# Optimization experiments

Measured on AMD Instinct MI355X. Metric: run time of the kernel, lower is better.

Reference implementation:

```python
import jax, jax.numpy as jnp
import numpy as np

C = 256
NUM_HEADS = 4
REDUCTION = 4
RED = C // REDUCTION           # 64
HEAD_DIM = RED // NUM_HEADS    # 16
SCALE = HEAD_DIM ** -0.5
LN_EPS = 1e-5


def setup_inputs() -> dict:
    key = jax.random.key(0)
    ks = jax.random.split(key, 9)
    B, H, W = 2, 64, 64
    x = jax.random.normal(ks[0], (B, C, H, W), dtype=jnp.float32)
    # LayerNorm params
    norm_w = jnp.ones((C,), jnp.float32)
    norm_b = jnp.zeros((C,), jnp.float32)
    # Linear weights (torch layout: [out, in]), y = x @ W.T
    qkv_w = jax.random.normal(ks[1], (3 * RED, C), jnp.float32) * (C ** -0.5)
    out_w = jax.random.normal(ks[2], (C, RED), jnp.float32) * (RED ** -0.5)
    # 1x1 conv weights, stored as [out_c, in_c]
    conv1_w = jax.random.normal(ks[3], (C // 2, C), jnp.float32) * (C ** -0.5)
    conv1_b = jax.random.normal(ks[4], (C // 2,), jnp.float32) * 0.01
    conv2_w = jax.random.normal(ks[5], (1, C // 2), jnp.float32) * ((C // 2) ** -0.5)
    conv2_b = jax.random.normal(ks[6], (1,), jnp.float32) * 0.01
    gamma = jnp.ones((1,), jnp.float32) * 0.5  # nonzero so output depends on attention
    return {"x": x, "norm_w": norm_w, "norm_b": norm_b, "qkv_w": qkv_w,
            "out_w": out_w, "conv1_w": conv1_w, "conv1_b": conv1_b,
            "conv2_w": conv2_w, "conv2_b": conv2_b, "gamma": gamma}


def reference(x, norm_w, norm_b, qkv_w, out_w, conv1_w, conv1_b, conv2_w, conv2_b, gamma):
    B, C_, H, W = x.shape
    N = H * W
    # [B, N, C]
    xf = x.reshape(B, C_, N).transpose(0, 2, 1)
    # LayerNorm over channel dim
    mu = jnp.mean(xf, axis=-1, keepdims=True)
    var = jnp.mean(jnp.square(xf - mu), axis=-1, keepdims=True)
    xn = (xf - mu) * jax.lax.rsqrt(var + LN_EPS) * norm_w + norm_b
    # QKV projection -> [B, N, 3*RED]
    qkv = jnp.einsum('bnc,oc->bno', xn, qkv_w)
    q, k, v = jnp.split(qkv, 3, axis=-1)
    def heads(t):  # [B, N, RED] -> [B, h, N, d]
        return t.reshape(B, N, NUM_HEADS, HEAD_DIM).transpose(0, 2, 1, 3)
    q, k, v = heads(q), heads(k), heads(v)
    attn = jax.nn.softmax(jnp.einsum('bhnd,bhmd->bhnm', q, k) * SCALE, axis=-1)
    # dynamic weight branch: two 1x1 convs on raw x
    d1 = jax.nn.relu(jnp.einsum('oc,bchw->bohw', conv1_w, x) + conv1_b[None, :, None, None])
    dyn = (jnp.einsum('oc,bchw->bohw', conv2_w, d1) + conv2_b[None, :, None, None])  # [B,1,H,W]
    dyn = dyn.reshape(B, 1, N)  # broadcast over heads
    # per-query row scaling of attention
    attn = attn * dyn[:, :, :, None]
    out = jnp.einsum('bhnm,bhmd->bhnd', attn, v)            # [B,h,N,d]
    out = out.transpose(0, 2, 1, 3).reshape(B, N, RED)      # [B,N,RED]
    out = jnp.einsum('bnr,cr->bnc', out, out_w)             # [B,N,C]
    out = out.transpose(0, 2, 1).reshape(B, C_, H, W)
    return jax.nn.sigmoid(gamma[0] * out + x)
```

## Files before the change

### kernel.cpp

```cpp
#include <hip/hip_runtime.h>
#include <cstdint>
#include <cstddef>

#define LOG2E 1.44269504088896340736f

typedef float  f32x16 __attribute__((ext_vector_type(16)));
typedef __bf16 bf16x8 __attribute__((ext_vector_type(8)));

union BF8 { bf16x8 v; uint u[4]; ushort us[8]; };

__device__ __forceinline__ uint pack_bf(float a, float b) {
    uint ua = __float_as_uint(a) + 0x8000u;
    uint ub = __float_as_uint(b) + 0x8000u;
    return __builtin_amdgcn_perm(ub, ua, 0x07060302u);
}
__device__ __forceinline__ float bf_lo(uint u) { return __uint_as_float(u << 16); }
__device__ __forceinline__ float bf_hi(uint u) { return __uint_as_float(u & 0xFFFF0000u); }

__global__ __launch_bounds__(256) void convert_w_kernel(
    const float* __restrict__ qkv_w, const float* __restrict__ c1w,
    const float* __restrict__ out_w,
    ushort* __restrict__ qkvw_b, ushort* __restrict__ c1w_b, ushort* __restrict__ ow_b)
{
    const int g = (blockIdx.x * 256 + threadIdx.x) * 4;
    const float* src; ushort* dst; int off; float sc = 1.f;
    if (g < 49152)      { src = qkv_w; dst = qkvw_b; off = g;
                          if (g < 16384) sc = 0.25f * LOG2E; }
    else if (g < 81920) { src = c1w;   dst = c1w_b;  off = g - 49152; }
    else                { src = out_w; dst = ow_b;   off = g - 81920; }
    float4 v = *(const float4*)(src + off);
    uint2 pk;
    pk.x = pack_bf(v.x * sc, v.y * sc);
    pk.y = pack_bf(v.z * sc, v.w * sc);
    *(uint2*)(dst + off) = pk;
}

__global__ __launch_bounds__(256) void ln_cast_kernel(
    const float* __restrict__ x, const float* __restrict__ nw, const float* __restrict__ nb,
    ushort* __restrict__ xnb, ushort* __restrict__ xrb)
{
    __shared__ uint  xp[32 * 144];
    __shared__ float red1[256], red2[256];
    __shared__ float muS[32], rsS[32];

    const int t  = threadIdx.x;
    const int b  = blockIdx.x >> 7;
    const int n0 = (blockIdx.x & 127) * 32;
    const int j  = t & 31;
    const int cg = t >> 5;
    const size_t xb = (size_t)b * 256 * 4096 + n0 + j;

    float v[32];
    #pragma unroll
    for (int i = 0; i < 32; ++i) v[i] = x[xb + (size_t)(cg * 32 + i) * 4096];
    float s1 = 0.f, s2 = 0.f;
    #pragma unroll
    for (int i = 0; i < 32; ++i) { s1 += v[i]; s2 += v[i] * v[i]; }
    #pragma unroll
    for (int i = 0; i < 16; ++i)
        xp[j * 144 + cg * 16 + i] = pack_bf(v[2 * i], v[2 * i + 1]);
    red1[t] = s1; red2[t] = s2;
    __syncthreads();
    if (t < 32) {
        float a = 0.f, q = 0.f;
        #pragma unroll
        for (int g2 = 0; g2 < 8; ++g2) { a += red1[g2 * 32 + t]; q += red2[g2 * 32 + t]; }
        float mu  = a * (1.f / 256.f);
        float var = q * (1.f / 256.f) - mu * mu;
        muS[t] = mu; rsS[t] = rsqrtf(fmaxf(var, 0.f) + 1e-5f);
    }
    __syncthreads();

    for (int it = 0; it < 4; ++it) {
        int lin = it * 256 + t;
        int px = lin >> 5, q = lin & 31;
        uint4 raw = *(uint4*)&xp[px * 144 + q * 4];
        size_t row = (size_t)blockIdx.x * 32 + px;
        *(uint4*)(xrb + row * 256 + q * 8) = raw;

        float mu = muS[px], rs = rsS[px];
        const float4 w0 = *(const float4*)(nw + q * 8);
        const float4 w1 = *(const float4*)(nw + q * 8 + 4);
        const float4 b0 = *(const float4*)(nb + q * 8);
        const float4 b1 = *(const float4*)(nb + q * 8 + 4);
        float e0 = (bf_lo(raw.x) - mu) * rs * w0.x + b0.x;
        float e1 = (bf_hi(raw.x) - mu) * rs * w0.y + b0.y;
        float e2 = (bf_lo(raw.y) - mu) * rs * w0.z + b0.z;
        float e3 = (bf_hi(raw.y) - mu) * rs * w0.w + b0.w;
        float e4 = (bf_lo(raw.z) - mu) * rs * w1.x + b1.x;
        float e5 = (bf_hi(raw.z) - mu) * rs * w1.y + b1.y;
        float e6 = (bf_lo(raw.w) - mu) * rs * w1.z + b1.z;
        float e7 = (bf_hi(raw.w) - mu) * rs * w1.w + b1.w;
        uint4 o;
        o.x = pack_bf(e0, e1); o.y = pack_bf(e2, e3);
        o.z = pack_bf(e4, e5); o.w = pack_bf(e6, e7);
        *(uint4*)(xnb + row * 256 + q * 8) = o;
    }
}

__global__ __launch_bounds__(256) void qkvconv_kernel(
    const ushort* __restrict__ xnb, const ushort* __restrict__ xrb,
    const ushort* __restrict__ qkvw_b, const ushort* __restrict__ c1w_b,
    const float* __restrict__ c1b, const float* __restrict__ c2w,
    const float* __restrict__ c2b,
    ushort* __restrict__ Qb, ushort* __restrict__ Kb, ushort* __restrict__ Vsw,
    float* __restrict__ dynb)
{
    __shared__ float trans[4][32 * 33];
    const int t    = threadIdx.x;
    const int w    = t >> 6;
    const int lane = t & 63;
    const int m    = lane & 31;
    const int h    = lane >> 5;
    const int pg   = blockIdx.x;
    const int b    = pg >> 7;
    const int n0   = (pg & 127) * 32;
    float* tr = trans[w];

    if (w < 3) {
        const ushort* bp  = xnb + ((size_t)pg * 32 + m) * 256 + h * 8;
        const ushort* ap0 = qkvw_b + ((size_t)(w * 64 + m)) * 256 + h * 8;
        const ushort* ap1 = ap0 + 32 * 256;
        f32x16 acc0, acc1;
        #pragma unroll
        for (int i = 0; i < 16; ++i) { acc0[i] = 0.f; acc1[i] = 0.f; }
        #pragma unroll 4
        for (int ks = 0; ks < 16; ++ks) {
            bf16x8 bf = *(const bf16x8*)(bp  + ks * 16);
            bf16x8 a0 = *(const bf16x8*)(ap0 + ks * 16);
            bf16x8 a1 = *(const bf16x8*)(ap1 + ks * 16);
            acc0 = __builtin_amdgcn_mfma_f32_32x32x16_bf16(a0, bf, acc0, 0, 0, 0);
            acc1 = __builtin_amdgcn_mfma_f32_32x32x16_bf16(a1, bf, acc1, 0, 0, 0);
        }
        for (int ti = 0; ti < 2; ++ti) {
            const f32x16& A = ti ? acc1 : acc0;
            #pragma unroll
            for (int r = 0; r < 16; ++r)
                tr[((r & 3) + 8 * (r >> 2) + 4 * h) * 33 + m] = A[r];
            if (w < 2) {
                ushort* dst = (w == 0) ? Qb : Kb;
                #pragma unroll
                for (int it = 0; it < 2; ++it) {
                    int unit = it * 2 + h;
                    int hl = unit >> 1, half = unit & 1;
                    float v0 = tr[(hl * 16 + half * 8 + 0) * 33 + m];
                    float v1 = tr[(hl * 16 + half * 8 + 1) * 33 + m];
                    float v2 = tr[(hl * 16 + half * 8 + 2) * 33 + m];
                    float v3 = tr[(hl * 16 + half * 8 + 3) * 33 + m];
                    float v4 = tr[(hl * 16 + half * 8 + 4) * 33 + m];
                    float v5 = tr[(hl * 16 + half * 8 + 5) * 33 + m];
                    float v6 = tr[(hl * 16 + half * 8 + 6) * 33 + m];
                    float v7 = tr[(hl * 16 + half * 8 + 7) * 33 + m];
                    uint4 pk;
                    pk.x = pack_bf(v0, v1); pk.y = pack_bf(v2, v3);
                    pk.z = pack_bf(v4, v5); pk.w = pack_bf(v6, v7);
                    int head = ti * 2 + hl;
                    *(uint4*)(dst + ((size_t)(b * 4 + head) * 4096 + n0 + m) * 16 + half * 8) = pk;
                }
            } else {
                int d = lane & 15, u = lane >> 4;
                #pragma unroll
                for (int it = 0; it < 4; ++it) {
                    int unit = it * 4 + u;
                    int hl = unit >> 3, sg = unit & 7;
                    float v0 = tr[(hl * 16 + d) * 33 + sg * 4 + 0];
                    float v1 = tr[(hl * 16 + d) * 33 + sg * 4 + 1];
                    float v2 = tr[(hl * 16 + d) * 33 + sg * 4 + 2];
                    float v3 = tr[(hl * 16 + d) * 33 + sg * 4 + 3];
                    uint2 pk; pk.x = pack_bf(v0, v1); pk.y = pack_bf(v2, v3);
                    int head = ti * 2 + hl;
                    *(uint2*)(Vsw + (((size_t)(b * 4 + head) * 1024 + (pg & 127) * 8 + sg) * 16 + d) * 4) = pk;
                }
            }
        }
    } else {
        const ushort* bp = xrb + ((size_t)pg * 32 + m) * 256 + h * 8;
        f32x16 acc[4];
        #pragma unroll
        for (int ti = 0; ti < 4; ++ti)
            #pragma unroll
            for (int i = 0; i < 16; ++i) acc[ti][i] = 0.f;
        #pragma unroll 2
        for (int ks = 0; ks < 16; ++ks) {
            bf16x8 bf = *(const bf16x8*)(bp + ks * 16);
            #pragma unroll
            for (int ti = 0; ti < 4; ++ti) {
                bf16x8 a = *(const bf16x8*)(c1w_b + ((size_t)(ti * 32 + m)) * 256 + ks * 16 + h * 8);
                acc[ti] = __builtin_amdgcn_mfma_f32_32x32x16_bf16(a, bf, acc[ti], 0, 0, 0);
            }
        }
        float partial = 0.f;
        for (int ti = 0; ti < 4; ++ti) {
            #pragma unroll
            for (int r = 0; r < 16; ++r)
                tr[((r & 3) + 8 * (r >> 2) + 4 * h) * 33 + m] = acc[ti][r];
            #pragma unroll
            for (int i = 0; i < 16; ++i) {
                int og = ti * 32 + h * 16 + i;
                partial += fmaxf(tr[(h * 16 + i) * 33 + m] + c1b[og], 0.f) * c2w[og];
            }
        }
        float tot = partial + __shfl_xor(partial, 32);
        if (lane < 32) dynb[(size_t)b * 4096 + n0 + m] = c2b[0] + tot;
    }
}

__global__ __launch_bounds__(256) void attn_kernel(
    const ushort* __restrict__ Qb, const ushort* __restrict__ Kb,
    const ushort* __restrict__ Vsw, float* __restrict__ AO2)
{
    const int t   = threadIdx.x;
    const int lid = t & 63;
    const int w   = t >> 6;
    const int c   = lid & 31;
    const int h   = lid >> 5;

    const int bi = blockIdx.x;
    const int kb = bi & 1;
    const int qb = (bi >> 1) & 31;
    const int bh = bi >> 6;
    const int nq = qb * 128 + w * 32;

    const bf16x8 qf = *(const bf16x8*)(Qb + ((size_t)bh * 4096 + nq + c) * 16 + h * 8);

    f32x16 oacc, zf;
    #pragma unroll
    for (int i = 0; i < 16; ++i) { oacc[i] = 0.f; zf[i] = 0.f; }

    const ushort* kp = Kb + ((size_t)bh * 4096 + kb * 2048 + c) * 16 + h * 8;
    const ushort* vb = Vsw + (size_t)bh * 65536 + ((size_t)kb * 512 + h) * 64 + c * 4;

    #pragma unroll 2
    for (int ch = 0; ch < 64; ++ch) {
        const bf16x8 kf = *(const bf16x8*)kp;
        f32x16 s = __builtin_amdgcn_mfma_f32_32x32x16_bf16(kf, qf, zf, 0, 0, 0);

        BF8 p1, p2;
        #pragma unroll
        for (int jj = 0; jj < 4; ++jj) {
            p1.u[jj] = pack_bf(__builtin_amdgcn_exp2f(s[2*jj]),   __builtin_amdgcn_exp2f(s[2*jj+1]));
            p2.u[jj] = pack_bf(__builtin_amdgcn_exp2f(s[8+2*jj]), __builtin_amdgcn_exp2f(s[8+2*jj+1]));
        }

        BF8 a1, a2;
        if (c < 16) {
            const uint2 g1 = *(const uint2*)(vb);
            const uint2 g2 = *(const uint2*)(vb + 128);
            const uint2 g3 = *(const uint2*)(vb + 256);
            const uint2 g4 = *(const uint2*)(vb + 384);
            a1.u[0] = g1.x; a1.u[1] = g1.y; a1.u[2] = g2.x; a1.u[3] = g2.y;
            a2.u[0] = g3.x; a2.u[1] = g3.y; a2.u[2] = g4.x; a2.u[3] = g4.y;
        } else {
            const uint f = (c == 16) ? 0x3F803F80u : 0u;
            a1.u[0] = a1.u[1] = a1.u[2] = a1.u[3] = f;
            a2.u[0] = a2.u[1] = a2.u[2] = a2.u[3] = f;
        }

        oacc = __builtin_amdgcn_mfma_f32_32x32x16_bf16(a1.v, p1.v, oacc, 0, 0, 0);
        oacc = __builtin_amdgcn_mfma_f32_32x32x16_bf16(a2.v, p2.v, oacc, 0, 0, 0);

        kp += 512; vb += 512;
    }

    float* ao = AO2 + ((size_t)(kb * 8 + bh) * 4096 + nq + c) * 20;
    float4 s0; s0.x = oacc[0]; s0.y = oacc[1]; s0.z = oacc[2]; s0.w = oacc[3];
    float4 s1; s1.x = oacc[4]; s1.y = oacc[5]; s1.z = oacc[6]; s1.w = oacc[7];
    *(float4*)(ao + 4 * h)     = s0;
    *(float4*)(ao + 8 + 4 * h) = s1;
    if (h == 0) ao[16] = oacc[8];
}

__global__ __launch_bounds__(256) void final_kernel(
    const float* __restrict__ AO2, const float* __restrict__ dynb,
    const ushort* __restrict__ ow_b, const float* __restrict__ x,
    const float* __restrict__ gamma, float* __restrict__ out)
{
    __shared__ float trans[4][32 * 33];
    const int t    = threadIdx.x;
    const int w    = t >> 6;
    const int lane = t & 63;
    const int m    = lane & 31;
    const int h    = lane >> 5;
    const int pg   = blockIdx.x;
    const int b    = pg >> 7;
    const int n0   = (pg & 127) * 32;
    float* tr = trans[w];

    const float dyn_px = dynb[(size_t)b * 4096 + n0 + m];
    const ushort* a0p = ow_b + ((size_t)(w * 64 + m)) * 64 + h * 8;
    const ushort* a1p = a0p + 32 * 64;

    f32x16 acc0, acc1;
    #pragma unroll
    for (int i = 0; i < 16; ++i) { acc0[i] = 0.f; acc1[i] = 0.f; }

    #pragma unroll
    for (int ks = 0; ks < 4; ++ks) {
        const float* r0 = AO2 + ((size_t)(b * 4 + ks) * 4096 + n0 + m) * 20;
        const float* r1 = r0 + (size_t)8 * 4096 * 20;
        float l   = r0[16] + r1[16];
        float fac = dyn_px / l;
        float4 u0 = *(const float4*)(r0 + h * 8);
        float4 u1 = *(const float4*)(r0 + h * 8 + 4);
        float4 t0 = *(const float4*)(r1 + h * 8);
        float4 t1 = *(const float4*)(r1 + h * 8 + 4);
        float e0 = (u0.x + t0.x) * fac, e1 = (u0.y + t0.y) * fac;
        float e2 = (u0.z + t0.z) * fac, e3 = (u0.w + t0.w) * fac;
        float e4 = (u1.x + t1.x) * fac, e5 = (u1.y + t1.y) * fac;
        float e6 = (u1.z + t1.z) * fac, e7 = (u1.w + t1.w) * fac;
        BF8 bfr;
        bfr.u[0] = pack_bf(e0, e1); bfr.u[1] = pack_bf(e2, e3);
        bfr.u[2] = pack_bf(e4, e5); bfr.u[3] = pack_bf(e6, e7);
        bf16x8 af0 = *(const bf16x8*)(a0p + ks * 16);
        bf16x8 af1 = *(const bf16x8*)(a1p + ks * 16);
        acc0 = __builtin_amdgcn_mfma_f32_32x32x16_bf16(af0, bfr.v, acc0, 0, 0, 0);
        acc1 = __builtin_amdgcn_mfma_f32_32x32x16_bf16(af1, bfr.v, acc1, 0, 0, 0);
    }

    const float g = gamma[0];
    for (int ti = 0; ti < 2; ++ti) {
        const f32x16& A = ti ? acc1 : acc0;
        #pragma unroll
        for (int r = 0; r < 16; ++r)
            tr[((r & 3) + 8 * (r >> 2) + 4 * h) * 33 + m] = A[r];
        int ob = w * 64 + ti * 32;
        #pragma unroll 4
        for (int it = 0; it < 16; ++it) {
            int o = it * 2 + h;
            float vv = tr[o * 33 + m];
            size_t idx = ((size_t)b * 256 + ob + o) * 4096 + n0 + m;
            float z = g * vv + x[idx];
            out[idx] = 1.f / (1.f + __builtin_amdgcn_exp2f(-z * LOG2E));
        }
    }
}

extern "C" void kernel_launch(void* const* d_in, const int* in_sizes, int n_in,
                              void* d_out, int out_size, void* d_ws, size_t ws_size,
                              hipStream_t stream)
{
    const float* x      = (const float*)d_in[0];
    const float* norm_w = (const float*)d_in[1];
    const float* norm_b = (const float*)d_in[2];
    const float* qkv_w  = (const float*)d_in[3];
    const float* out_w  = (const float*)d_in[4];
    const float* c1w    = (const float*)d_in[5];
    const float* c1b    = (const float*)d_in[6];
    const float* c2w    = (const float*)d_in[7];
    const float* c2b    = (const float*)d_in[8];
    const float* gamma  = (const float*)d_in[9];

    char* ws = (char*)d_ws;
    ushort* Qb     = (ushort*)ws;
    ushort* Kb     = Qb + 524288;
    ushort* Vsw    = Kb + 524288;
    ushort* qkvw_b = Vsw + 524288;
    ushort* c1w_b  = qkvw_b + 49152;
    ushort* ow_b   = c1w_b + 32768;
    float*  dynb   = (float*)(ws + 3342336);
    ushort* xnb    = (ushort*)(ws + 3375104);
    ushort* xrb    = xnb + 2097152;
    float*  AO2    = (float*)(ws + 3375104);

    hipLaunchKernelGGL(convert_w_kernel, dim3(96), dim3(256), 0, stream,
                       qkv_w, c1w, out_w, qkvw_b, c1w_b, ow_b);
    hipLaunchKernelGGL(ln_cast_kernel, dim3(256), dim3(256), 0, stream,
                       x, norm_w, norm_b, xnb, xrb);
    hipLaunchKernelGGL(qkvconv_kernel, dim3(256), dim3(256), 0, stream,
                       xnb, xrb, qkvw_b, c1w_b, c1b, c2w, c2b, Qb, Kb, Vsw, dynb);
    hipLaunchKernelGGL(attn_kernel, dim3(512), dim3(256), 0, stream,
                       Qb, Kb, Vsw, AO2);
    hipLaunchKernelGGL(final_kernel, dim3(256), dim3(256), 0, stream,
                       AO2, dynb, ow_b, x, gamma, (float*)d_out);
}
```

Before: 139.3 us.

## Fold weight conversion into LN kernel, split qkvconv into single-wave blocks, truncate P packing

Weight-to-bf16 conversion now runs in extra blocks appended to the LayerNorm/cast kernel, removing one kernel launch. The qkv/conv kernel is restructured from 256-thread blocks with four role-specialized waves into 1024 single-wave blocks, each taking one role, to spread work across more CUs. Attention probabilities are packed to bf16 by truncation instead of round-to-nearest, saving ALU work in the inner loop. The truncation adds a small downward bias in the softmax numerators.

```diff
diff --git a/kernel.cpp b/kernel.cpp
--- a/kernel.cpp
+++ b/kernel.cpp
@@ -14,38 +14,42 @@
     uint ub = __float_as_uint(b) + 0x8000u;
     return __builtin_amdgcn_perm(ub, ua, 0x07060302u);
 }
+__device__ __forceinline__ uint pack_bf_trunc(float a, float b) {
+    return __builtin_amdgcn_perm(__float_as_uint(b), __float_as_uint(a), 0x07060302u);
+}
 __device__ __forceinline__ float bf_lo(uint u) { return __uint_as_float(u << 16); }
 __device__ __forceinline__ float bf_hi(uint u) { return __uint_as_float(u & 0xFFFF0000u); }
 
-__global__ __launch_bounds__(256) void convert_w_kernel(
-    const float* __restrict__ qkv_w, const float* __restrict__ c1w,
-    const float* __restrict__ out_w,
-    ushort* __restrict__ qkvw_b, ushort* __restrict__ c1w_b, ushort* __restrict__ ow_b)
-{
-    const int g = (blockIdx.x * 256 + threadIdx.x) * 4;
-    const float* src; ushort* dst; int off; float sc = 1.f;
-    if (g < 49152)      { src = qkv_w; dst = qkvw_b; off = g;
-                          if (g < 16384) sc = 0.25f * LOG2E; }
-    else if (g < 81920) { src = c1w;   dst = c1w_b;  off = g - 49152; }
-    else                { src = out_w; dst = ow_b;   off = g - 81920; }
-    float4 v = *(const float4*)(src + off);
-    uint2 pk;
-    pk.x = pack_bf(v.x * sc, v.y * sc);
-    pk.y = pack_bf(v.z * sc, v.w * sc);
-    *(uint2*)(dst + off) = pk;
-}
-
 __global__ __launch_bounds__(256) void ln_cast_kernel(
     const float* __restrict__ x, const float* __restrict__ nw, const float* __restrict__ nb,
-    ushort* __restrict__ xnb, ushort* __restrict__ xrb)
+    const float* __restrict__ qkv_w, const float* __restrict__ c1w, const float* __restrict__ out_w,
+    ushort* __restrict__ xnb, ushort* __restrict__ xrb,
+    ushort* __restrict__ qkvw_b, ushort* __restrict__ c1w_b, ushort* __restrict__ ow_b)
 {
     __shared__ uint  xp[32 * 144];
     __shared__ float red1[256], red2[256];
     __shared__ float muS[32], rsS[32];
 
     const int t  = threadIdx.x;
-    const int b  = blockIdx.x >> 7;
-    const int n0 = (blockIdx.x & 127) * 32;
+    const int bi = blockIdx.x;
+
+    if (bi >= 256) {
+        const int g = ((bi - 256) * 256 + t) * 4;
+        const float* src; ushort* dst; int off; float sc = 1.f;
+        if (g < 49152)      { src = qkv_w; dst = qkvw_b; off = g;
+                              if (g < 16384) sc = 0.25f * LOG2E; }
+        else if (g < 81920) { src = c1w;   dst = c1w_b;  off = g - 49152; }
+        else                { src = out_w; dst = ow_b;   off = g - 81920; }
+        float4 v = *(const float4*)(src + off);
+        uint2 pk;
+        pk.x = pack_bf(v.x * sc, v.y * sc);
+        pk.y = pack_bf(v.z * sc, v.w * sc);
+        *(uint2*)(dst + off) = pk;
+        return;
+    }
+
+    const int b  = bi >> 7;
+    const int n0 = (bi & 127) * 32;
     const int j  = t & 31;
     const int cg = t >> 5;
     const size_t xb = (size_t)b * 256 * 4096 + n0 + j;
@@ -75,7 +79,7 @@
         int lin = it * 256 + t;
         int px = lin >> 5, q = lin & 31;
         uint4 raw = *(uint4*)&xp[px * 144 + q * 4];
-        size_t row = (size_t)blockIdx.x * 32 + px;
+        size_t row = (size_t)bi * 32 + px;
         *(uint4*)(xrb + row * 256 + q * 8) = raw;
 
         float mu = muS[px], rs = rsS[px];
@@ -98,7 +102,7 @@
     }
 }
 
-__global__ __launch_bounds__(256) void qkvconv_kernel(
+__global__ __launch_bounds__(64) void qkvconv_kernel(
     const ushort* __restrict__ xnb, const ushort* __restrict__ xrb,
     const ushort* __restrict__ qkvw_b, const ushort* __restrict__ c1w_b,
     const float* __restrict__ c1b, const float* __restrict__ c2w,
@@ -106,20 +110,19 @@
     ushort* __restrict__ Qb, ushort* __restrict__ Kb, ushort* __restrict__ Vsw,
     float* __restrict__ dynb)
 {
-    __shared__ float trans[4][32 * 33];
-    const int t    = threadIdx.x;
-    const int w    = t >> 6;
-    const int lane = t & 63;
-    const int m    = lane & 31;
-    const int h    = lane >> 5;
-    const int pg   = blockIdx.x;
-    const int b    = pg >> 7;
-    const int n0   = (pg & 127) * 32;
-    float* tr = trans[w];
-
-    if (w < 3) {
+    __shared__ float tr[32 * 33];
+    const int t  = threadIdx.x;
+    const int m  = t & 31;
+    const int h  = t >> 5;
+    const int bi = blockIdx.x;
+    const int j  = bi & 3;
+    const int pg = bi >> 2;
+    const int b  = pg >> 7;
+    const int n0 = (pg & 127) * 32;
+
+    if (j < 3) {
         const ushort* bp  = xnb + ((size_t)pg * 32 + m) * 256 + h * 8;
-        const ushort* ap0 = qkvw_b + ((size_t)(w * 64 + m)) * 256 + h * 8;
+        const ushort* ap0 = qkvw_b + ((size_t)(j * 64 + m)) * 256 + h * 8;
         const ushort* ap1 = ap0 + 32 * 256;
         f32x16 acc0, acc1;
         #pragma unroll
@@ -137,8 +140,8 @@
             #pragma unroll
             for (int r = 0; r < 16; ++r)
                 tr[((r & 3) + 8 * (r >> 2) + 4 * h) * 33 + m] = A[r];
-            if (w < 2) {
-                ushort* dst = (w == 0) ? Qb : Kb;
+            if (j < 2) {
+                ushort* dst = (j == 0) ? Qb : Kb;
                 #pragma unroll
                 for (int it = 0; it < 2; ++it) {
                     int unit = it * 2 + h;
@@ -158,7 +161,7 @@
                     *(uint4*)(dst + ((size_t)(b * 4 + head) * 4096 + n0 + m) * 16 + half * 8) = pk;
                 }
             } else {
-                int d = lane & 15, u = lane >> 4;
+                int d = t & 15, u = t >> 4;
                 #pragma unroll
                 for (int it = 0; it < 4; ++it) {
                     int unit = it * 4 + u;
@@ -201,7 +204,7 @@
             }
         }
         float tot = partial + __shfl_xor(partial, 32);
-        if (lane < 32) dynb[(size_t)b * 4096 + n0 + m] = c2b[0] + tot;
+        if (t < 32) dynb[(size_t)b * 4096 + n0 + m] = c2b[0] + tot;
     }
 }
 
@@ -238,8 +241,8 @@
         BF8 p1, p2;
         #pragma unroll
         for (int jj = 0; jj < 4; ++jj) {
-            p1.u[jj] = pack_bf(__builtin_amdgcn_exp2f(s[2*jj]),   __builtin_amdgcn_exp2f(s[2*jj+1]));
-            p2.u[jj] = pack_bf(__builtin_amdgcn_exp2f(s[8+2*jj]), __builtin_amdgcn_exp2f(s[8+2*jj+1]));
+            p1.u[jj] = pack_bf_trunc(__builtin_amdgcn_exp2f(s[2*jj]),   __builtin_amdgcn_exp2f(s[2*jj+1]));
+            p2.u[jj] = pack_bf_trunc(__builtin_amdgcn_exp2f(s[8+2*jj]), __builtin_amdgcn_exp2f(s[8+2*jj+1]));
         }
 
         BF8 a1, a2;
@@ -362,11 +365,9 @@
     ushort* xrb    = xnb + 2097152;
     float*  AO2    = (float*)(ws + 3375104);
 
-    hipLaunchKernelGGL(convert_w_kernel, dim3(96), dim3(256), 0, stream,
-                       qkv_w, c1w, out_w, qkvw_b, c1w_b, ow_b);
-    hipLaunchKernelGGL(ln_cast_kernel, dim3(256), dim3(256), 0, stream,
-                       x, norm_w, norm_b, xnb, xrb);
-    hipLaunchKernelGGL(qkvconv_kernel, dim3(256), dim3(256), 0, stream,
+    hipLaunchKernelGGL(ln_cast_kernel, dim3(352), dim3(256), 0, stream,
+                       x, norm_w, norm_b, qkv_w, c1w, out_w, xnb, xrb, qkvw_b, c1w_b, ow_b);
+    hipLaunchKernelGGL(qkvconv_kernel, dim3(1024), dim3(64), 0, stream,
                        xnb, xrb, qkvw_b, c1w_b, c1b, c2w, c2b, Qb, Kb, Vsw, dynb);
     hipLaunchKernelGGL(attn_kernel, dim3(512), dim3(256), 0, stream,
                        Qb, Kb, Vsw, AO2);
```

New measurement: 141.6 us. Within noise of the previous version (+1.6%).

## Fuse weight conversion, LayerNorm and QKV/conv projections into one pre-kernel

Applied to the files above, without the earlier changes.

Merges the weight-conversion, LayerNorm/cast and QKV/conv1 projection kernels into a single kernel. Normalized and raw activations stay in shared memory instead of a global round trip, and fp32 weights are converted to bf16 on the fly inside the MFMA loops, including in the final kernel. This removes two launches and the intermediate global buffers, at the cost of redundant per-block weight conversion and larger fp32 weight loads. The attention softmax also switches to truncating bf16 packing to save an add per element.

```diff
diff --git a/kernel.cpp b/kernel.cpp
--- a/kernel.cpp
+++ b/kernel.cpp
@@ -14,124 +14,103 @@
     uint ub = __float_as_uint(b) + 0x8000u;
     return __builtin_amdgcn_perm(ub, ua, 0x07060302u);
 }
-__device__ __forceinline__ float bf_lo(uint u) { return __uint_as_float(u << 16); }
-__device__ __forceinline__ float bf_hi(uint u) { return __uint_as_float(u & 0xFFFF0000u); }
-
-__global__ __launch_bounds__(256) void convert_w_kernel(
+__device__ __forceinline__ uint pack_bf_trunc(float a, float b) {
+    return __builtin_amdgcn_perm(__float_as_uint(b), __float_as_uint(a), 0x07060302u);
+}
+
+__global__ __launch_bounds__(256) void fused_pre_kernel(
+    const float* __restrict__ x, const float* __restrict__ nw, const float* __restrict__ nb,
     const float* __restrict__ qkv_w, const float* __restrict__ c1w,
-    const float* __restrict__ out_w,
-    ushort* __restrict__ qkvw_b, ushort* __restrict__ c1w_b, ushort* __restrict__ ow_b)
-{
-    const int g = (blockIdx.x * 256 + threadIdx.x) * 4;
-    const float* src; ushort* dst; int off; float sc = 1.f;
-    if (g < 49152)      { src = qkv_w; dst = qkvw_b; off = g;
-                          if (g < 16384) sc = 0.25f * LOG2E; }
-    else if (g < 81920) { src = c1w;   dst = c1w_b;  off = g - 49152; }
-    else                { src = out_w; dst = ow_b;   off = g - 81920; }
-    float4 v = *(const float4*)(src + off);
-    uint2 pk;
-    pk.x = pack_bf(v.x * sc, v.y * sc);
-    pk.y = pack_bf(v.z * sc, v.w * sc);
-    *(uint2*)(dst + off) = pk;
-}
-
-__global__ __launch_bounds__(256) void ln_cast_kernel(
-    const float* __restrict__ x, const float* __restrict__ nw, const float* __restrict__ nb,
-    ushort* __restrict__ xnb, ushort* __restrict__ xrb)
-{
-    __shared__ uint  xp[32 * 144];
-    __shared__ float red1[256], red2[256];
-    __shared__ float muS[32], rsS[32];
-
-    const int t  = threadIdx.x;
-    const int b  = blockIdx.x >> 7;
-    const int n0 = (blockIdx.x & 127) * 32;
-    const int j  = t & 31;
-    const int cg = t >> 5;
-    const size_t xb = (size_t)b * 256 * 4096 + n0 + j;
-
-    float v[32];
-    #pragma unroll
-    for (int i = 0; i < 32; ++i) v[i] = x[xb + (size_t)(cg * 32 + i) * 4096];
-    float s1 = 0.f, s2 = 0.f;
-    #pragma unroll
-    for (int i = 0; i < 32; ++i) { s1 += v[i]; s2 += v[i] * v[i]; }
-    #pragma unroll
-    for (int i = 0; i < 16; ++i)
-        xp[j * 144 + cg * 16 + i] = pack_bf(v[2 * i], v[2 * i + 1]);
-    red1[t] = s1; red2[t] = s2;
-    __syncthreads();
-    if (t < 32) {
-        float a = 0.f, q = 0.f;
-        #pragma unroll
-        for (int g2 = 0; g2 < 8; ++g2) { a += red1[g2 * 32 + t]; q += red2[g2 * 32 + t]; }
-        float mu  = a * (1.f / 256.f);
-        float var = q * (1.f / 256.f) - mu * mu;
-        muS[t] = mu; rsS[t] = rsqrtf(fmaxf(var, 0.f) + 1e-5f);
-    }
-    __syncthreads();
-
-    for (int it = 0; it < 4; ++it) {
-        int lin = it * 256 + t;
-        int px = lin >> 5, q = lin & 31;
-        uint4 raw = *(uint4*)&xp[px * 144 + q * 4];
-        size_t row = (size_t)blockIdx.x * 32 + px;
-        *(uint4*)(xrb + row * 256 + q * 8) = raw;
-
-        float mu = muS[px], rs = rsS[px];
-        const float4 w0 = *(const float4*)(nw + q * 8);
-        const float4 w1 = *(const float4*)(nw + q * 8 + 4);
-        const float4 b0 = *(const float4*)(nb + q * 8);
-        const float4 b1 = *(const float4*)(nb + q * 8 + 4);
-        float e0 = (bf_lo(raw.x) - mu) * rs * w0.x + b0.x;
-        float e1 = (bf_hi(raw.x) - mu) * rs * w0.y + b0.y;
-        float e2 = (bf_lo(raw.y) - mu) * rs * w0.z + b0.z;
-        float e3 = (bf_hi(raw.y) - mu) * rs * w0.w + b0.w;
-        float e4 = (bf_lo(raw.z) - mu) * rs * w1.x + b1.x;
-        float e5 = (bf_hi(raw.z) - mu) * rs * w1.y + b1.y;
-        float e6 = (bf_lo(raw.w) - mu) * rs * w1.z + b1.z;
-        float e7 = (bf_hi(raw.w) - mu) * rs * w1.w + b1.w;
-        uint4 o;
-        o.x = pack_bf(e0, e1); o.y = pack_bf(e2, e3);
-        o.z = pack_bf(e4, e5); o.w = pack_bf(e6, e7);
-        *(uint4*)(xnb + row * 256 + q * 8) = o;
-    }
-}
-
-__global__ __launch_bounds__(256) void qkvconv_kernel(
-    const ushort* __restrict__ xnb, const ushort* __restrict__ xrb,
-    const ushort* __restrict__ qkvw_b, const ushort* __restrict__ c1w_b,
-    const float* __restrict__ c1b, const float* __restrict__ c2w,
-    const float* __restrict__ c2b,
+    const float* __restrict__ c1b, const float* __restrict__ c2w, const float* __restrict__ c2b,
     ushort* __restrict__ Qb, ushort* __restrict__ Kb, ushort* __restrict__ Vsw,
     float* __restrict__ dynb)
 {
+    __shared__ uint  xpn[32 * 144];
+    __shared__ uint  xpr[32 * 144];
     __shared__ float trans[4][32 * 33];
-    const int t    = threadIdx.x;
+    __shared__ float red1[256], red2[256];
+    __shared__ float muS[32], rsS[32];
+    __shared__ float nwS[256], nbS[256];
+
+    const int t  = threadIdx.x;
+    const int pg = blockIdx.x;
+    const int b  = pg >> 7;
+    const int n0 = (pg & 127) * 32;
+
+    {
+        const int j  = t & 31;
+        const int cg = t >> 5;
+        const size_t xb = (size_t)b * 256 * 4096 + n0 + j;
+        nwS[t] = nw[t]; nbS[t] = nb[t];
+
+        float v[32];
+        #pragma unroll
+        for (int i = 0; i < 32; ++i) v[i] = x[xb + (size_t)(cg * 32 + i) * 4096];
+        float s1 = 0.f, s2 = 0.f;
+        #pragma unroll
+        for (int i = 0; i < 32; ++i) { s1 += v[i]; s2 += v[i] * v[i]; }
+        #pragma unroll
+        for (int i = 0; i < 16; ++i)
+            xpr[j * 144 + cg * 16 + i] = pack_bf(v[2 * i], v[2 * i + 1]);
+        red1[t] = s1; red2[t] = s2;
+        __syncthreads();
+        if (t < 32) {
+            float a = 0.f, q = 0.f;
+            #pragma unroll
+            for (int g2 = 0; g2 < 8; ++g2) { a += red1[g2 * 32 + t]; q += red2[g2 * 32 + t]; }
+            float mu  = a * (1.f / 256.f);
+            float var = q * (1.f / 256.f) - mu * mu;
+            muS[t] = mu; rsS[t] = rsqrtf(fmaxf(var, 0.f) + 1e-5f);
+        }
+        __syncthreads();
+        float mu = muS[j], rs = rsS[j];
+        #pragma unroll
+        for (int i = 0; i < 16; ++i) {
+            int c0 = cg * 32 + 2 * i;
+            float e0 = (v[2 * i]     - mu) * rs * nwS[c0]     + nbS[c0];
+            float e1 = (v[2 * i + 1] - mu) * rs * nwS[c0 + 1] + nbS[c0 + 1];
+            xpn[j * 144 + cg * 16 + i] = pack_bf(e0, e1);
+        }
+        __syncthreads();
+    }
+
     const int w    = t >> 6;
     const int lane = t & 63;
     const int m    = lane & 31;
     const int h    = lane >> 5;
-    const int pg   = blockIdx.x;
-    const int b    = pg >> 7;
-    const int n0   = (pg & 127) * 32;
     float* tr = trans[w];
 
     if (w < 3) {
-        const ushort* bp  = xnb + ((size_t)pg * 32 + m) * 256 + h * 8;
-        const ushort* ap0 = qkvw_b + ((size_t)(w * 64 + m)) * 256 + h * 8;
-        const ushort* ap1 = ap0 + 32 * 256;
+        const uint*  bp  = xpn + m * 144 + h * 4;
+        const float* w0p = qkv_w + (size_t)(w * 64 + m) * 256 + h * 8;
+        const float* w1p = w0p + 32 * 256;
+        const float sc = (w == 0) ? (0.25f * LOG2E) : 1.f;
+
         f32x16 acc0, acc1;
         #pragma unroll
         for (int i = 0; i < 16; ++i) { acc0[i] = 0.f; acc1[i] = 0.f; }
+
         #pragma unroll 4
         for (int ks = 0; ks < 16; ++ks) {
-            bf16x8 bf = *(const bf16x8*)(bp  + ks * 16);
-            bf16x8 a0 = *(const bf16x8*)(ap0 + ks * 16);
-            bf16x8 a1 = *(const bf16x8*)(ap1 + ks * 16);
-            acc0 = __builtin_amdgcn_mfma_f32_32x32x16_bf16(a0, bf, acc0, 0, 0, 0);
-            acc1 = __builtin_amdgcn_mfma_f32_32x32x16_bf16(a1, bf, acc1, 0, 0, 0);
-        }
+            uint4 bu = *(const uint4*)(bp + ks * 8);
+            BF8 bfr; bfr.u[0] = bu.x; bfr.u[1] = bu.y; bfr.u[2] = bu.z; bfr.u[3] = bu.w;
+            float4 a00 = *(const float4*)(w0p + ks * 16);
+            float4 a01 = *(const float4*)(w0p + ks * 16 + 4);
+            float4 a10 = *(const float4*)(w1p + ks * 16);
+            float4 a11 = *(const float4*)(w1p + ks * 16 + 4);
+            BF8 af0, af1;
+            af0.u[0] = pack_bf(a00.x * sc, a00.y * sc);
+            af0.u[1] = pack_bf(a00.z * sc, a00.w * sc);
+            af0.u[2] = pack_bf(a01.x * sc, a01.y * sc);
+            af0.u[3] = pack_bf(a01.z * sc, a01.w * sc);
+            af1.u[0] = pack_bf(a10.x * sc, a10.y * sc);
+            af1.u[1] = pack_bf(a10.z * sc, a10.w * sc);
+            af1.u[2] = pack_bf(a11.x * sc, a11.y * sc);
+            af1.u[3] = pack_bf(a11.z * sc, a11.w * sc);
+            acc0 = __builtin_amdgcn_mfma_f32_32x32x16_bf16(af0.v, bfr.v, acc0, 0, 0, 0);
+            acc1 = __builtin_amdgcn_mfma_f32_32x32x16_bf16(af1.v, bfr.v, acc1, 0, 0, 0);
+        }
+
         for (int ti = 0; ti < 2; ++ti) {
             const f32x16& A = ti ? acc1 : acc0;
             #pragma unroll
@@ -174,7 +153,7 @@
             }
         }
     } else {
-        const ushort* bp = xrb + ((size_t)pg * 32 + m) * 256 + h * 8;
+        const uint* bp = xpr + m * 144 + h * 4;
         f32x16 acc[4];
         #pragma unroll
         for (int ti = 0; ti < 4; ++ti)
@@ -182,11 +161,17 @@
             for (int i = 0; i < 16; ++i) acc[ti][i] = 0.f;
         #pragma unroll 2
         for (int ks = 0; ks < 16; ++ks) {
-            bf16x8 bf = *(const bf16x8*)(bp + ks * 16);
+            uint4 bu = *(const uint4*)(bp + ks * 8);
+            BF8 bfr; bfr.u[0] = bu.x; bfr.u[1] = bu.y; bfr.u[2] = bu.z; bfr.u[3] = bu.w;
             #pragma unroll
             for (int ti = 0; ti < 4; ++ti) {
-                bf16x8 a = *(const bf16x8*)(c1w_b + ((size_t)(ti * 32 + m)) * 256 + ks * 16 + h * 8);
-                acc[ti] = __builtin_amdgcn_mfma_f32_32x32x16_bf16(a, bf, acc[ti], 0, 0, 0);
+                const float* wp = c1w + (size_t)(ti * 32 + m) * 256 + ks * 16 + h * 8;
+                float4 a0 = *(const float4*)(wp);
+                float4 a1 = *(const float4*)(wp + 4);
+                BF8 af;
+                af.u[0] = pack_bf(a0.x, a0.y); af.u[1] = pack_bf(a0.z, a0.w);
+                af.u[2] = pack_bf(a1.x, a1.y); af.u[3] = pack_bf(a1.z, a1.w);
+                acc[ti] = __builtin_amdgcn_mfma_f32_32x32x16_bf16(af.v, bfr.v, acc[ti], 0, 0, 0);
             }
         }
         float partial = 0.f;
@@ -238,8 +223,8 @@
         BF8 p1, p2;
         #pragma unroll
         for (int jj = 0; jj < 4; ++jj) {
-            p1.u[jj] = pack_bf(__builtin_amdgcn_exp2f(s[2*jj]),   __builtin_amdgcn_exp2f(s[2*jj+1]));
-            p2.u[jj] = pack_bf(__builtin_amdgcn_exp2f(s[8+2*jj]), __builtin_amdgcn_exp2f(s[8+2*jj+1]));
+            p1.u[jj] = pack_bf_trunc(__builtin_amdgcn_exp2f(s[2*jj]),   __builtin_amdgcn_exp2f(s[2*jj+1]));
+            p2.u[jj] = pack_bf_trunc(__builtin_amdgcn_exp2f(s[8+2*jj]), __builtin_amdgcn_exp2f(s[8+2*jj+1]));
         }
 
         BF8 a1, a2;
@@ -272,7 +257,7 @@
 
 __global__ __launch_bounds__(256) void final_kernel(
     const float* __restrict__ AO2, const float* __restrict__ dynb,
-    const ushort* __restrict__ ow_b, const float* __restrict__ x,
+    const float* __restrict__ out_w, const float* __restrict__ x,
     const float* __restrict__ gamma, float* __restrict__ out)
 {
     __shared__ float trans[4][32 * 33];
@@ -287,8 +272,8 @@
     float* tr = trans[w];
 
     const float dyn_px = dynb[(size_t)b * 4096 + n0 + m];
-    const ushort* a0p = ow_b + ((size_t)(w * 64 + m)) * 64 + h * 8;
-    const ushort* a1p = a0p + 32 * 64;
+    const float* a0p = out_w + (size_t)(w * 64 + m) * 64 + h * 8;
+    const float* a1p = a0p + 32 * 64;
 
     f32x16 acc0, acc1;
     #pragma unroll
@@ -311,10 +296,19 @@
         BF8 bfr;
         bfr.u[0] = pack_bf(e0, e1); bfr.u[1] = pack_bf(e2, e3);
         bfr.u[2] = pack_bf(e4, e5); bfr.u[3] = pack_bf(e6, e7);
-        bf16x8 af0 = *(const bf16x8*)(a0p + ks * 16);
-        bf16x8 af1 = *(const bf16x8*)(a1p + ks * 16);
-        acc0 = __builtin_amdgcn_mfma_f32_32x32x16_bf16(af0, bfr.v, acc0, 0, 0, 0);
-        acc1 = __builtin_amdgcn_mfma_f32_32x32x16_bf16(af1, bfr.v, acc1, 0, 0, 0);
+
+        float4 f00 = *(const float4*)(a0p + ks * 16);
+        float4 f01 = *(const float4*)(a0p + ks * 16 + 4);
+        float4 f10 = *(const float4*)(a1p + ks * 16);
+        float4 f11 = *(const float4*)(a1p + ks * 16 + 4);
+        BF8 af0, af1;
+        af0.u[0] = pack_bf(f00.x, f00.y); af0.u[1] = pack_bf(f00.z, f00.w);
+        af0.u[2] = pack_bf(f01.x, f01.y); af0.u[3] = pack_bf(f01.z, f01.w);
+        af1.u[0] = pack_bf(f10.x, f10.y); af1.u[1] = pack_bf(f10.z, f10.w);
+        af1.u[2] = pack_bf(f11.x, f11.y); af1.u[3] = pack_bf(f11.z, f11.w);
+
+        acc0 = __builtin_amdgcn_mfma_f32_32x32x16_bf16(af0.v, bfr.v, acc0, 0, 0, 0);
+        acc1 = __builtin_amdgcn_mfma_f32_32x32x16_bf16(af1.v, bfr.v, acc1, 0, 0, 0);
     }
 
     const float g = gamma[0];
@@ -351,25 +345,16 @@
     const float* gamma  = (const float*)d_in[9];
 
     char* ws = (char*)d_ws;
-    ushort* Qb     = (ushort*)ws;
-    ushort* Kb     = Qb + 524288;
-    ushort* Vsw    = Kb + 524288;
-    ushort* qkvw_b = Vsw + 524288;
-    ushort* c1w_b  = qkvw_b + 49152;
-    ushort* ow_b   = c1w_b + 32768;
-    float*  dynb   = (float*)(ws + 3342336);
-    ushort* xnb    = (ushort*)(ws + 3375104);
-    ushort* xrb    = xnb + 2097152;
-    float*  AO2    = (float*)(ws + 3375104);
-
-    hipLaunchKernelGGL(convert_w_kernel, dim3(96), dim3(256), 0, stream,
-                       qkv_w, c1w, out_w, qkvw_b, c1w_b, ow_b);
-    hipLaunchKernelGGL(ln_cast_kernel, dim3(256), dim3(256), 0, stream,
-                       x, norm_w, norm_b, xnb, xrb);
-    hipLaunchKernelGGL(qkvconv_kernel, dim3(256), dim3(256), 0, stream,
-                       xnb, xrb, qkvw_b, c1w_b, c1b, c2w, c2b, Qb, Kb, Vsw, dynb);
+    ushort* Qb   = (ushort*)ws;
+    ushort* Kb   = Qb + 524288;
+    ushort* Vsw  = Kb + 524288;
+    float*  dynb = (float*)(ws + 3145728);
+    float*  AO2  = (float*)(ws + 3178496);
+
+    hipLaunchKernelGGL(fused_pre_kernel, dim3(256), dim3(256), 0, stream,
+                       x, norm_w, norm_b, qkv_w, c1w, c1b, c2w, c2b, Qb, Kb, Vsw, dynb);
     hipLaunchKernelGGL(attn_kernel, dim3(512), dim3(256), 0, stream,
                        Qb, Kb, Vsw, AO2);
     hipLaunchKernelGGL(final_kernel, dim3(256), dim3(256), 0, stream,
-                       AO2, dynb, ow_b, x, gamma, (float*)d_out);
-}
+                       AO2, dynb, out_w, x, gamma, (float*)d_out);
+}
```

Result: no change. 140.4 us (+0.8%).
